# Optimization experiments

Measured on AMD Instinct MI355X. Metric: run time of the kernel, lower is better.

Reference implementation:

```python
import jax, jax.numpy as jnp
import numpy as np
from jax import lax

H = 64
W = 64
NUM_HEADS = 8
SR = 4


def setup_inputs() -> dict:
    key = jax.random.key(0)
    ks = jax.random.split(key, 6)
    B, N, C = 16, H * W, 256
    x = jax.random.normal(ks[0], (B, N, C), jnp.float32)
    Wq = jax.random.normal(ks[1], (C, C), jnp.float32) * (C ** -0.5)
    Wkv = jax.random.normal(ks[2], (C, 2 * C), jnp.float32) * (C ** -0.5)
    sr_w = jax.random.normal(ks[3], (C, C, SR, SR), jnp.float32) * ((C * SR * SR) ** -0.5)
    sr_b = jnp.zeros((C,), jnp.float32)
    ln_g = jnp.ones((C,), jnp.float32)
    ln_b = jnp.zeros((C,), jnp.float32)
    Wp = jax.random.normal(ks[4], (C, C), jnp.float32) * (C ** -0.5)
    bp = jnp.zeros((C,), jnp.float32)
    return {"x": x, "Wq": Wq, "Wkv": Wkv, "sr_w": sr_w, "sr_b": sr_b,
            "ln_g": ln_g, "ln_b": ln_b, "Wp": Wp, "bp": bp}


def _layernorm(x, g, b, eps=1e-5):
    mu = jnp.mean(x, axis=-1, keepdims=True)
    var = jnp.var(x, axis=-1, keepdims=True)
    return (x - mu) * lax.rsqrt(var + eps) * g + b


def reference(x, Wq, Wkv, sr_w, sr_b, ln_g, ln_b, Wp, bp):
    B, N, C = x.shape
    h, hd = NUM_HEADS, C // NUM_HEADS
    scale = hd ** -0.5

    # q: [B, h, N, hd]
    q = (x @ Wq).reshape(B, N, h, hd).transpose(0, 2, 1, 3)

    # spatial reduction of KV: conv stride SR on (B, C, H, W)
    x_ = x.transpose(0, 2, 1).reshape(B, C, H, W)
    x_ = lax.conv_general_dilated(
        x_, sr_w, window_strides=(SR, SR), padding='VALID',
        dimension_numbers=('NCHW', 'OIHW', 'NCHW')) + sr_b[None, :, None, None]
    x_ = x_.reshape(B, C, -1).transpose(0, 2, 1)  # [B, M, C], M = (H/SR)*(W/SR)
    x_ = _layernorm(x_, ln_g, ln_b)

    M = x_.shape[1]
    kv = (x_ @ Wkv).reshape(B, M, 2, h, hd)
    k = kv[:, :, 0].transpose(0, 2, 1, 3)  # [B, h, M, hd]
    v = kv[:, :, 1].transpose(0, 2, 1, 3)

    attn = jnp.einsum('bhnd,bhmd->bhnm', q, k) * scale
    attn = jax.nn.softmax(attn, axis=-1)
    out = jnp.einsum('bhnm,bhmd->bhnd', attn, v)
    out = out.transpose(0, 2, 1, 3).reshape(B, N, C)
    return out @ Wp + bp
```

## Files before the change

kernel.cpp:

```cpp
#include <hip/hip_runtime.h>
#include <hip/hip_bf16.h>
#include <math.h>
#include <stdint.h>


typedef float f32x4 __attribute__((ext_vector_type(4)));
typedef short bf16x8 __attribute__((ext_vector_type(8)));
typedef short bf16x4v __attribute__((ext_vector_type(4)));

#define QSCALE (0.17677669529663687f * 1.4426950408889634f)

__device__ inline unsigned short f2bf(float f) {
  __hip_bfloat16 h = __float2bfloat16(f);
  union { __hip_bfloat16 h; unsigned short u; } c;
  c.h = h;
  return c.u;
}

__device__ inline float fast_exp2(float x) {
#if __has_builtin(__builtin_amdgcn_exp2f)
  return __builtin_amdgcn_exp2f(x);
#else
  return __expf(x * 0.6931471805599453f);
#endif
}

__global__ __launch_bounds__(256) void prep_wT_all(
    const float* __restrict__ Wq, const float* __restrict__ Wp,
    const float* __restrict__ Wkv, unsigned short* __restrict__ WqT,
    unsigned short* __restrict__ WpT, unsigned short* __restrict__ WkvT) {
  int k = blockIdx.x, y = blockIdx.y, n = threadIdx.x;
  if (y == 0) {
    WqT[n * 256 + k] = f2bf(Wq[(size_t)k * 256 + n] * QSCALE);
  } else if (y == 1) {
    WpT[n * 256 + k] = f2bf(Wp[(size_t)k * 256 + n]);
  } else {
    int nn = (y - 2) * 256 + n;
    WkvT[nn * 256 + k] = f2bf(Wkv[(size_t)k * 512 + nn]);
  }
}

__global__ __launch_bounds__(256) void prep_srwT(const float* __restrict__ srw,
                                                 unsigned short* __restrict__ o) {
  int oc = blockIdx.x, t = threadIdx.x;
  const float* src = srw + (size_t)oc * 4096 + t * 16;
  f32x4 v[4];
#pragma unroll
  for (int j = 0; j < 4; ++j) v[j] = *(const f32x4*)(src + j * 4);
  unsigned short* dst = o + (size_t)oc * 4096 + t;
#pragma unroll
  for (int pp = 0; pp < 16; ++pp) dst[pp * 256] = f2bf(v[pp >> 2][pp & 3]);
}

template <int BM, int BN, int GATHER, int AFP32, int OUTBF, int BIAS>
__global__ __launch_bounds__(256) void gemm_bf16(
    const void* __restrict__ Av, const unsigned short* __restrict__ BT,
    const float* __restrict__ bias, void* __restrict__ Cout,
    int M, int N, int K, int CHUNK) {
  constexpr int AISS = BM / 32, BISS = BN / 32;
  constexpr int WM = BM / 2, WN = BN / 2, FM = WM / 16, FN = WN / 16;
  __shared__ unsigned short As[BM * 64];
  __shared__ unsigned short Bs[BN * 64];
  const int t = threadIdx.x;
  const int bm0 = blockIdx.x * BM, bn0 = blockIdx.y * BN;
  const int kz = blockIdx.z;
  const int k0b = kz * CHUNK;
  const int k0e = (k0b + CHUNK < K) ? (k0b + CHUNK) : K;
  const int w = t >> 6, lane = t & 63, g = lane >> 4, li = lane & 15;
  const int wr = w >> 1, wc = w & 1;
  const int srow = t >> 3, scol = (t & 7) * 8;

  f32x4 acc[FM][FN];
#pragma unroll
  for (int mi = 0; mi < FM; ++mi)
#pragma unroll
    for (int ni = 0; ni < FN; ++ni) acc[mi][ni] = (f32x4){0.f, 0.f, 0.f, 0.f};

  for (int k0 = k0b; k0 < k0e; k0 += 64) {
    bf16x8 areg[AISS], breg[BISS];
#pragma unroll
    for (int j = 0; j < AISS; ++j) {
      int r = j * 32 + srow;
      size_t eoff;
      if constexpr (GATHER) {
        int grow = bm0 + r;
        int bb = grow >> 8, rem = grow & 255;
        int oy = rem >> 4, ox = rem & 15;
        int kg = k0 + scol;
        int pos = kg >> 8, c = kg & 255;
        int ky = pos >> 2, kx = pos & 3;
        eoff = ((size_t)(bb * 4096 + (4 * oy + ky) * 64 + 4 * ox + kx)) * 256 + c;
      } else {
        eoff = (size_t)(bm0 + r) * K + k0 + scol;
      }
      if constexpr (AFP32) {
        const float* srcf = (const float*)Av + eoff;
        f32x4 lo = *(const f32x4*)srcf;
        f32x4 hi = *(const f32x4*)(srcf + 4);
#pragma unroll
        for (int e = 0; e < 4; ++e) {
          areg[j][e] = (short)f2bf(lo[e]);
          areg[j][e + 4] = (short)f2bf(hi[e]);
        }
      } else {
        areg[j] = *(const bf16x8*)((const unsigned short*)Av + eoff);
      }
    }
#pragma unroll
    for (int j = 0; j < BISS; ++j)
      breg[j] = *(const bf16x8*)(BT + (size_t)(bn0 + j * 32 + srow) * K + k0 + scol);
    __syncthreads();
#pragma unroll
    for (int j = 0; j < AISS; ++j) *(bf16x8*)&As[(j * 32 + srow) * 64 + scol] = areg[j];
#pragma unroll
    for (int j = 0; j < BISS; ++j) *(bf16x8*)&Bs[(j * 32 + srow) * 64 + scol] = breg[j];
    __syncthreads();
#pragma unroll
    for (int kc = 0; kc < 64; kc += 32) {
      bf16x8 af[FM], bfr[FN];
#pragma unroll
      for (int mi = 0; mi < FM; ++mi)
        af[mi] = *(const bf16x8*)&As[(wr * WM + mi * 16 + li) * 64 + kc + g * 8];
#pragma unroll
      for (int ni = 0; ni < FN; ++ni)
        bfr[ni] = *(const bf16x8*)&Bs[(wc * WN + ni * 16 + li) * 64 + kc + g * 8];
#pragma unroll
      for (int mi = 0; mi < FM; ++mi)
#pragma unroll
        for (int ni = 0; ni < FN; ++ni)
          acc[mi][ni] = __builtin_amdgcn_mfma_f32_16x16x32_bf16(af[mi], bfr[ni],
                                                               acc[mi][ni], 0, 0, 0);
    }
  }
#pragma unroll
  for (int mi = 0; mi < FM; ++mi) {
    int row = bm0 + wr * WM + mi * 16 + 4 * g;
#pragma unroll
    for (int ni = 0; ni < FN; ++ni) {
      int col = bn0 + wc * WN + ni * 16 + li;
      f32x4 v = acc[mi][ni];
      if constexpr (BIAS) {
        float bb = bias[col];
        v[0] += bb; v[1] += bb; v[2] += bb; v[3] += bb;
      }
      if constexpr (OUTBF) {
        unsigned short* C = (unsigned short*)Cout + (size_t)kz * M * N;
#pragma unroll
        for (int r = 0; r < 4; ++r) C[(size_t)(row + r) * N + col] = f2bf(v[r]);
      } else {
        float* C = (float*)Cout + (size_t)kz * M * N;
#pragma unroll
        for (int r = 0; r < 4; ++r) C[(size_t)(row + r) * N + col] = v[r];
      }
    }
  }
}

__global__ __launch_bounds__(256) void ln4_kernel(const float* __restrict__ xrp,
                                                  const float* __restrict__ srb,
                                                  const float* __restrict__ g,
                                                  const float* __restrict__ bta,
                                                  unsigned short* __restrict__ out) {
  const int row = blockIdx.x * 4 + (threadIdx.x >> 6);
  const int lane = threadIdx.x & 63;
  const size_t off = (size_t)row * 256 + lane * 4;
  const size_t CH = (size_t)4096 * 256;
  f32x4 v = *(const f32x4*)(xrp + off);
  v += *(const f32x4*)(xrp + CH + off);
  v += *(const f32x4*)(xrp + 2 * CH + off);
  v += *(const f32x4*)(xrp + 3 * CH + off);
  v += *(const f32x4*)&srb[lane * 4];
  float s = v[0] + v[1] + v[2] + v[3];
  float sq = v[0] * v[0] + v[1] * v[1] + v[2] * v[2] + v[3] * v[3];
#pragma unroll
  for (int o = 32; o > 0; o >>= 1) {
    s += __shfl_xor(s, o);
    sq += __shfl_xor(sq, o);
  }
  float mean = s * (1.0f / 256.0f);
  float var = sq * (1.0f / 256.0f) - mean * mean;
  float rstd = rsqrtf(var + 1e-5f);
  f32x4 gv = *(const f32x4*)&g[lane * 4];
  f32x4 bv = *(const f32x4*)&bta[lane * 4];
  bf16x4v o;
#pragma unroll
  for (int j = 0; j < 4; ++j) o[j] = (short)f2bf((v[j] - mean) * rstd * gv[j] + bv[j]);
  *(bf16x4v*)&out[(size_t)row * 256 + lane * 4] = o;
}

__global__ __launch_bounds__(256) void attn_mfma(const unsigned short* __restrict__ qbf,
                                                 const unsigned short* __restrict__ kvbf,
                                                 unsigned short* __restrict__ obf) {
  __shared__ unsigned short Ks[256 * 40];
  __shared__ unsigned short Vt2[32 * 264];
  const int t = threadIdx.x;
  const int idx = blockIdx.x;
  const int bh = idx >> 4, nblk = idx & 15;
  const int b = bh >> 3, h = bh & 7;
  {
    const unsigned short* kp = kvbf + ((size_t)(b * 256 + t)) * 512 + h * 32;
    bf16x8 kr[4], vr[4];
#pragma unroll
    for (int j = 0; j < 4; ++j) kr[j] = *(const bf16x8*)(kp + j * 8);
#pragma unroll
    for (int j = 0; j < 4; ++j) vr[j] = *(const bf16x8*)(kp + 256 + j * 8);
#pragma unroll
    for (int j = 0; j < 4; ++j) *(bf16x8*)&Ks[t * 40 + j * 8] = kr[j];
    const int m = t;
    const int pcol = (m & ~31) + ((m >> 2) & 3) * 8 + (m & 3) + 4 * ((m >> 4) & 1);
#pragma unroll
    for (int j = 0; j < 4; ++j)
#pragma unroll
      for (int e = 0; e < 8; ++e) Vt2[(j * 8 + e) * 264 + pcol] = (unsigned short)vr[j][e];
  }
  __syncthreads();
  const int w = t >> 6, lane = t & 63, g = lane >> 4, li = lane & 15;
  const int nbase = nblk * 256 + w * 64;
#pragma unroll 1
  for (int nt = 0; nt < 4; ++nt) {
    const int nrow = nbase + nt * 16 + li;
    bf16x8 qf = *(const bf16x8*)(qbf + ((size_t)(b * 4096 + nrow)) * 256 + h * 32 + g * 8);
    f32x4 zero = {0.f, 0.f, 0.f, 0.f};
    f32x4 st[16];
    float sm[16];
#pragma unroll
    for (int mt = 0; mt < 16; ++mt) {
      bf16x8 kf = *(const bf16x8*)&Ks[(mt * 16 + li) * 40 + g * 8];
      st[mt] = __builtin_amdgcn_mfma_f32_16x16x32_bf16(kf, qf, zero, 0, 0, 0);
    }
#pragma unroll
    for (int mt = 0; mt < 16; ++mt) {
      f32x4 p;
#pragma unroll
      for (int r = 0; r < 4; ++r) p[r] = fast_exp2(st[mt][r]);
      st[mt] = p;
      sm[mt] = (p[0] + p[1]) + (p[2] + p[3]);
    }
#pragma unroll
    for (int s = 8; s > 0; s >>= 1)
#pragma unroll
      for (int i = 0; i < 8; ++i)
        if (i < s) sm[i] += sm[i + s];
    float l = sm[0];
    l += __shfl_xor(l, 16);
    l += __shfl_xor(l, 32);
    const float rl = 1.0f / l;
    bf16x8 pb[8];
#pragma unroll
    for (int c = 0; c < 8; ++c)
#pragma unroll
      for (int e = 0; e < 4; ++e) {
        pb[c][e] = (short)f2bf(st[2 * c][e]);
        pb[c][e + 4] = (short)f2bf(st[2 * c + 1][e]);
      }
#pragma unroll
    for (int dt = 0; dt < 2; ++dt) {
      f32x4 acc = {0.f, 0.f, 0.f, 0.f};
      const int drow = (dt * 16 + li) * 264;
#pragma unroll
      for (int c = 0; c < 8; ++c) {
        bf16x8 vf = *(const bf16x8*)&Vt2[drow + c * 32 + g * 8];
        acc = __builtin_amdgcn_mfma_f32_16x16x32_bf16(vf, pb[c], acc, 0, 0, 0);
      }
      unsigned short* op = obf + ((size_t)(b * 4096 + nbase + nt * 16 + li)) * 256 +
                           h * 32 + dt * 16 + 4 * g;
      bf16x4v ov;
#pragma unroll
      for (int r = 0; r < 4; ++r) ov[r] = (short)f2bf(acc[r] * rl);
      *(bf16x4v*)op = ov;
    }
  }
}

extern "C" void kernel_launch(void* const* d_in, const int* in_sizes, int n_in,
                              void* d_out, int out_size, void* d_ws, size_t ws_size,
                              hipStream_t stream) {
  const float* x   = (const float*)d_in[0];
  const float* Wq  = (const float*)d_in[1];
  const float* Wkv = (const float*)d_in[2];
  const float* srw = (const float*)d_in[3];
  const float* srb = (const float*)d_in[4];
  const float* lng = (const float*)d_in[5];
  const float* lnb = (const float*)d_in[6];
  const float* Wp  = (const float*)d_in[7];
  const float* bp  = (const float*)d_in[8];
  float* out = (float*)d_out;

  char* wsc = (char*)d_ws;
  unsigned short* qbf   = (unsigned short*)(wsc);
  unsigned short* abf   = (unsigned short*)(wsc + 33554432);
  float*          xrp   = (float*)(wsc + 67108864);
  unsigned short* xlnbf = (unsigned short*)(wsc + 83886080);
  unsigned short* kvb   = (unsigned short*)(wsc + 85983232);
  unsigned short* wqT   = (unsigned short*)(wsc + 90177536);
  unsigned short* wpT   = (unsigned short*)(wsc + 90308608);
  unsigned short* wkvT  = (unsigned short*)(wsc + 90439680);
  unsigned short* srwT  = (unsigned short*)(wsc + 90701824);

  prep_wT_all<<<dim3(256, 4), 256, 0, stream>>>(Wq, Wp, Wkv, wqT, wpT, wkvT);
  prep_srwT<<<256, 256, 0, stream>>>(srw, srwT);
  gemm_bf16<128, 128, 0, 1, 1, 0><<<dim3(512, 2), 256, 0, stream>>>(
      x, wqT, nullptr, qbf, 65536, 256, 256, 256);
  gemm_bf16<64, 64, 1, 1, 0, 0><<<dim3(64, 4, 4), 256, 0, stream>>>(
      x, srwT, nullptr, xrp, 4096, 256, 4096, 1024);
  ln4_kernel<<<1024, 256, 0, stream>>>(xrp, srb, lng, lnb, xlnbf);
  gemm_bf16<64, 64, 0, 0, 1, 0><<<dim3(64, 8), 256, 0, stream>>>(
      xlnbf, wkvT, nullptr, kvb, 4096, 512, 256, 256);
  attn_mfma<<<2048, 256, 0, stream>>>(qbf, kvb, abf);
  gemm_bf16<128, 128, 0, 0, 0, 1><<<dim3(512, 2), 256, 0, stream>>>(
      abf, wpT, bp, out, 65536, 256, 256, 256);
}
```

Before: 244.7 us.

## Prefetch A tiles across k-steps and fuse Q projection with SR conv launch

The GEMM body now prefetches the next A tile into registers while the current tile's MFMAs run, with a compile-time trip count and fully unrolled double-buffered phases. The Q projection and the spatial-reduction conv GEMM are merged into one launch that dispatches by block index, so the two independent GEMMs can run concurrently and fill the GPU. Output-projection and Q GEMMs switch from 128x128 to 128x64 tiles for more blocks. The extra register buffers raise register pressure and may lower occupancy.

```diff
diff --git a/kernel.cpp b/kernel.cpp
--- a/kernel.cpp
+++ b/kernel.cpp
@@ -52,20 +52,18 @@
   for (int pp = 0; pp < 16; ++pp) dst[pp * 256] = f2bf(v[pp >> 2][pp & 3]);
 }
 
-template <int BM, int BN, int GATHER, int AFP32, int OUTBF, int BIAS>
-__global__ __launch_bounds__(256) void gemm_bf16(
+template <int BM, int BN, int NITER, int GATHER, int AFP32, int OUTBF, int BIAS>
+__device__ __forceinline__ void gemm_body(
     const void* __restrict__ Av, const unsigned short* __restrict__ BT,
     const float* __restrict__ bias, void* __restrict__ Cout,
-    int M, int N, int K, int CHUNK) {
+    int M, int N, int K, int bxi, int byi, int kz, char* smem) {
   constexpr int AISS = BM / 32, BISS = BN / 32;
   constexpr int WM = BM / 2, WN = BN / 2, FM = WM / 16, FN = WN / 16;
-  __shared__ unsigned short As[BM * 64];
-  __shared__ unsigned short Bs[BN * 64];
+  unsigned short* As = (unsigned short*)smem;
+  unsigned short* Bs = As + BM * 64;
   const int t = threadIdx.x;
-  const int bm0 = blockIdx.x * BM, bn0 = blockIdx.y * BN;
-  const int kz = blockIdx.z;
-  const int k0b = kz * CHUNK;
-  const int k0e = (k0b + CHUNK < K) ? (k0b + CHUNK) : K;
+  const int bm0 = bxi * BM, bn0 = byi * BN;
+  const int k0b = kz * (NITER * 64);
   const int w = t >> 6, lane = t & 63, g = lane >> 4, li = lane & 15;
   const int wr = w >> 1, wc = w & 1;
   const int srow = t >> 3, scol = (t & 7) * 8;
@@ -76,45 +74,63 @@
 #pragma unroll
     for (int ni = 0; ni < FN; ++ni) acc[mi][ni] = (f32x4){0.f, 0.f, 0.f, 0.f};
 
-  for (int k0 = k0b; k0 < k0e; k0 += 64) {
-    bf16x8 areg[AISS], breg[BISS];
+  f32x4 araw0[AISS][2], araw1[AISS][2];
+  bf16x8 areg0[AISS], areg1[AISS];
+
+  auto aoff = [&](int j, int k0) -> size_t {
+    int r = j * 32 + srow;
+    if constexpr (GATHER) {
+      int grow = bm0 + r;
+      int bb = grow >> 8, rem = grow & 255;
+      int oy = rem >> 4, ox = rem & 15;
+      int kg = k0 + scol;
+      int pos = kg >> 8, c = kg & 255;
+      int ky = pos >> 2, kx = pos & 3;
+      return ((size_t)(bb * 4096 + (4 * oy + ky) * 64 + 4 * ox + kx)) * 256 + c;
+    } else {
+      return (size_t)(bm0 + r) * K + k0 + scol;
+    }
+  };
+
+  auto loadA = [&](int k0, f32x4 (*araw)[2], bf16x8* areg) {
 #pragma unroll
     for (int j = 0; j < AISS; ++j) {
-      int r = j * 32 + srow;
-      size_t eoff;
-      if constexpr (GATHER) {
-        int grow = bm0 + r;
-        int bb = grow >> 8, rem = grow & 255;
-        int oy = rem >> 4, ox = rem & 15;
-        int kg = k0 + scol;
-        int pos = kg >> 8, c = kg & 255;
-        int ky = pos >> 2, kx = pos & 3;
-        eoff = ((size_t)(bb * 4096 + (4 * oy + ky) * 64 + 4 * ox + kx)) * 256 + c;
+      size_t e = aoff(j, k0);
+      if constexpr (AFP32) {
+        const float* s = (const float*)Av + e;
+        araw[j][0] = *(const f32x4*)s;
+        araw[j][1] = *(const f32x4*)(s + 4);
       } else {
-        eoff = (size_t)(bm0 + r) * K + k0 + scol;
-      }
-      if constexpr (AFP32) {
-        const float* srcf = (const float*)Av + eoff;
-        f32x4 lo = *(const f32x4*)srcf;
-        f32x4 hi = *(const f32x4*)(srcf + 4);
-#pragma unroll
-        for (int e = 0; e < 4; ++e) {
-          areg[j][e] = (short)f2bf(lo[e]);
-          areg[j][e + 4] = (short)f2bf(hi[e]);
-        }
-      } else {
-        areg[j] = *(const bf16x8*)((const unsigned short*)Av + eoff);
-      }
-    }
+        areg[j] = *(const bf16x8*)((const unsigned short*)Av + e);
+      }
+    }
+  };
+
+  auto phase = [&](int k0, f32x4 (*araw)[2], bf16x8* areg,
+                   int nk0, f32x4 (*nraw)[2], bf16x8* nareg, bool pf) {
+    bf16x8 breg[BISS];
 #pragma unroll
     for (int j = 0; j < BISS; ++j)
       breg[j] = *(const bf16x8*)(BT + (size_t)(bn0 + j * 32 + srow) * K + k0 + scol);
     __syncthreads();
 #pragma unroll
-    for (int j = 0; j < AISS; ++j) *(bf16x8*)&As[(j * 32 + srow) * 64 + scol] = areg[j];
+    for (int j = 0; j < AISS; ++j) {
+      bf16x8 v;
+      if constexpr (AFP32) {
+#pragma unroll
+        for (int e = 0; e < 4; ++e) {
+          v[e] = (short)f2bf(araw[j][0][e]);
+          v[e + 4] = (short)f2bf(araw[j][1][e]);
+        }
+      } else {
+        v = areg[j];
+      }
+      *(bf16x8*)&As[(j * 32 + srow) * 64 + scol] = v;
+    }
 #pragma unroll
     for (int j = 0; j < BISS; ++j) *(bf16x8*)&Bs[(j * 32 + srow) * 64 + scol] = breg[j];
     __syncthreads();
+    if (pf) loadA(nk0, nraw, nareg);
 #pragma unroll
     for (int kc = 0; kc < 64; kc += 32) {
       bf16x8 af[FM], bfr[FN];
@@ -131,7 +147,16 @@
           acc[mi][ni] = __builtin_amdgcn_mfma_f32_16x16x32_bf16(af[mi], bfr[ni],
                                                                acc[mi][ni], 0, 0, 0);
     }
-  }
+  };
+
+  loadA(k0b, araw0, areg0);
+#pragma unroll
+  for (int i = 0; i < NITER; i += 2) {
+    phase(k0b + i * 64, araw0, areg0, k0b + (i + 1) * 64, araw1, areg1, i + 1 < NITER);
+    phase(k0b + (i + 1) * 64, araw1, areg1, k0b + (i + 2) * 64, araw0, areg0,
+          i + 2 < NITER);
+  }
+
 #pragma unroll
   for (int mi = 0; mi < FM; ++mi) {
     int row = bm0 + wr * WM + mi * 16 + 4 * g;
@@ -153,6 +178,31 @@
         for (int r = 0; r < 4; ++r) C[(size_t)(row + r) * N + col] = v[r];
       }
     }
+  }
+}
+
+template <int BM, int BN, int NITER, int GATHER, int AFP32, int OUTBF, int BIAS>
+__global__ __launch_bounds__(256) void gemm_bf16(
+    const void* __restrict__ Av, const unsigned short* __restrict__ BT,
+    const float* __restrict__ bias, void* __restrict__ Cout, int M, int N, int K) {
+  extern __shared__ char smem[];
+  gemm_body<BM, BN, NITER, GATHER, AFP32, OUTBF, BIAS>(
+      Av, BT, bias, Cout, M, N, K, blockIdx.x, blockIdx.y, blockIdx.z, smem);
+}
+
+__global__ __launch_bounds__(256) void qconv_kernel(
+    const float* __restrict__ x, const unsigned short* __restrict__ wqT,
+    const unsigned short* __restrict__ srwT, unsigned short* __restrict__ qbf,
+    float* __restrict__ xrp) {
+  extern __shared__ char smem[];
+  int bid = blockIdx.x;
+  if (bid < 1024) {
+    gemm_body<64, 64, 16, 1, 1, 0, 0>(x, srwT, nullptr, xrp, 4096, 256, 4096,
+                                      bid & 63, (bid >> 6) & 3, bid >> 8, smem);
+  } else {
+    int r = bid - 1024;
+    gemm_body<128, 64, 4, 0, 1, 1, 0>(x, wqT, nullptr, qbf, 65536, 256, 256,
+                                      r >> 2, r & 3, 0, smem);
   }
 }
 
@@ -299,14 +349,11 @@
 
   prep_wT_all<<<dim3(256, 4), 256, 0, stream>>>(Wq, Wp, Wkv, wqT, wpT, wkvT);
   prep_srwT<<<256, 256, 0, stream>>>(srw, srwT);
-  gemm_bf16<128, 128, 0, 1, 1, 0><<<dim3(512, 2), 256, 0, stream>>>(
-      x, wqT, nullptr, qbf, 65536, 256, 256, 256);
-  gemm_bf16<64, 64, 1, 1, 0, 0><<<dim3(64, 4, 4), 256, 0, stream>>>(
-      x, srwT, nullptr, xrp, 4096, 256, 4096, 1024);
+  qconv_kernel<<<3072, 256, 24576, stream>>>(x, wqT, srwT, qbf, xrp);
   ln4_kernel<<<1024, 256, 0, stream>>>(xrp, srb, lng, lnb, xlnbf);
-  gemm_bf16<64, 64, 0, 0, 1, 0><<<dim3(64, 8), 256, 0, stream>>>(
-      xlnbf, wkvT, nullptr, kvb, 4096, 512, 256, 256);
+  gemm_bf16<64, 64, 4, 0, 0, 1, 0><<<dim3(64, 8), 256, 16384, stream>>>(
+      xlnbf, wkvT, nullptr, kvb, 4096, 512, 256);
   attn_mfma<<<2048, 256, 0, stream>>>(qbf, kvb, abf);
-  gemm_bf16<128, 128, 0, 0, 0, 1><<<dim3(512, 2), 256, 0, stream>>>(
-      abf, wpT, bp, out, 65536, 256, 256, 256);
-}
+  gemm_bf16<128, 64, 4, 0, 0, 0, 1><<<dim3(512, 4), 256, 24576, stream>>>(
+      abf, wpT, bp, out, 65536, 256, 256);
+}
```

After: 259.7 us. +6.1%, slower.
